# Kernel tuning notes

Measured on AMD Instinct MI355X. Metric: run time of the kernel, lower is better.

## Reference

```python
import jax, jax.numpy as jnp
import numpy as np

NEG_SLOPE = 0.2
EPS = 1e-16

N_NODES = 32768
N_EDGES = 160000
DIM = 768
HEADS1 = 4
OUT1 = DIM // HEADS1  # 192 per head, concat -> 768
HEADS2 = 1
OUT2 = DIM
N_REL = 3


def setup_inputs() -> dict:
    key = jax.random.key(0)
    ks = jax.random.split(key, 12)
    s = 0.02
    return {
        "x": jax.random.normal(ks[0], (N_NODES, DIM), dtype=jnp.float32),
        "edge_index": jax.random.randint(ks[1], (2, N_EDGES), 0, N_NODES, dtype=jnp.int64),
        "edge_type": jax.random.randint(ks[2], (N_EDGES,), 0, N_REL, dtype=jnp.int64),
        "W1": jax.random.normal(ks[3], (N_REL, DIM, HEADS1 * OUT1), dtype=jnp.float32) * s,
        "q1": jax.random.normal(ks[4], (HEADS1 * OUT1, HEADS1), dtype=jnp.float32) * s,
        "k1": jax.random.normal(ks[5], (HEADS1 * OUT1, HEADS1), dtype=jnp.float32) * s,
        "b1": jnp.zeros((HEADS1 * OUT1,), dtype=jnp.float32),
        "W2": jax.random.normal(ks[6], (N_REL, DIM, HEADS2 * OUT2), dtype=jnp.float32) * s,
        "q2": jax.random.normal(ks[7], (HEADS2 * OUT2, HEADS2), dtype=jnp.float32) * s,
        "k2": jax.random.normal(ks[8], (HEADS2 * OUT2, HEADS2), dtype=jnp.float32) * s,
        "b2": jnp.zeros((HEADS2 * OUT2,), dtype=jnp.float32),
    }


def rgat_conv(x, W, q, k, b, src, dst, etype, heads, out_ch, n_nodes):
    """PyG RGATConv, additive-self-attention, across-relation, concat=True, eval mode."""
    # per-relation transform of all nodes: [R, N, H*O] (avoids [E, in, H*O] weight gather)
    xr = jnp.einsum('nd,rdf->rnf', x, W)
    oi = xr[etype, dst]                      # [E, H*O] transformed target feats
    oj = xr[etype, src]                      # [E, H*O] transformed source feats
    qi = oi @ q                              # [E, H]
    kj = oj @ k                              # [E, H]
    alpha = jax.nn.leaky_relu(qi + kj, NEG_SLOPE)
    # segment softmax over edges sharing the same target node
    m = jax.ops.segment_max(alpha, dst, num_segments=n_nodes)     # [N, H]
    e = jnp.exp(alpha - m[dst])
    z = jax.ops.segment_sum(e, dst, num_segments=n_nodes)         # [N, H]
    a = e / (z[dst] + EPS)                                        # [E, H]
    msg = (a[:, :, None] * oj.reshape(-1, heads, out_ch)).reshape(-1, heads * out_ch)
    out = jax.ops.segment_sum(msg, dst, num_segments=n_nodes)     # [N, H*O]
    return out + b


def reference(x, edge_index, edge_type, W1, q1, k1, b1, W2, q2, k2, b2):
    src, dst = edge_index[0], edge_index[1]
    n = x.shape[0]
    h = rgat_conv(x, W1, q1, k1, b1, src, dst, edge_type, HEADS1, OUT1, n)
    h = jax.nn.elu(h)
    # dropout is identity in eval mode
    out = rgat_conv(h, W2, q2, k2, b2, src, dst, edge_type, HEADS2, OUT2, n)
    return out
```

## Files before the change

### kernel.cpp

```cpp
#include <hip/hip_runtime.h>


#define DIM   768
#define NREL  3

typedef __bf16 bf16x8 __attribute__((ext_vector_type(8)));
typedef float  f32x4  __attribute__((ext_vector_type(4)));
typedef unsigned short us4 __attribute__((ext_vector_type(4)));
typedef unsigned short us8 __attribute__((ext_vector_type(8)));

__device__ __forceinline__ float bfs(unsigned short u){
  union { unsigned u; float f; } v; v.u = ((unsigned)u) << 16; return v.f;
}
__device__ __forceinline__ float bfl(unsigned x){
  union { unsigned u; float f; } v; v.u = x << 16; return v.f;
}
__device__ __forceinline__ float bfh(unsigned x){
  union { unsigned u; float f; } v; v.u = x & 0xffff0000u; return v.f;
}
__device__ __forceinline__ unsigned short f2bf(float f){
  union { float f; unsigned u; } v; v.f = f;
  unsigned r = v.u + 0x7fffu + ((v.u >> 16) & 1u);
  return (unsigned short)(r >> 16);
}
__device__ __forceinline__ unsigned pck(float a, float b){
  return (unsigned)f2bf(a) | ((unsigned)f2bf(b) << 16);
}
__device__ __forceinline__ float ldf(const void* p, size_t i, int is32){
  return is32 ? ((const float*)p)[i] : bfs(((const unsigned short*)p)[i]);
}
__device__ __forceinline__ int ldi(const void* p, size_t i, int is64){
  return is64 ? ((const int*)p)[2 * i] : ((const int*)p)[i];
}

typedef __attribute__((address_space(1))) void gvoid_t;
typedef __attribute__((address_space(3))) void lvoid_t;
__device__ __forceinline__ void gload16(const void* g, void* l){
  __builtin_amdgcn_global_load_lds((gvoid_t*)g, (lvoid_t*)l, 16, 0, 0);
}

template<int H>
__device__ __forceinline__ float sel(const float (&a)[H], int h){
  float v = a[0];
#pragma unroll
  for (int i = 1; i < H; ++i) v = (h == i) ? a[i] : v;
  return v;
}

__global__ void detect_kernel(const unsigned short* __restrict__ xu,
                              const unsigned* __restrict__ eiu,
                              const unsigned* __restrict__ etyu,
                              int* __restrict__ flags){
  __shared__ int s_weird, s_ei, s_ety;
  int t = threadIdx.x;
  if (t == 0){ s_weird = 0; s_ei = 0; s_ety = 0; }
  __syncthreads();
  unsigned short u = xu[2 * t];
  int ex = (u >> 7) & 0xff;
  if (ex >= 0xF0 || ex <= 0x40) atomicAdd(&s_weird, 1);
  if (t < 128){
    if (eiu[2 * t + 1]  != 0) atomicAdd(&s_ei, 1);
    if (etyu[2 * t + 1] != 0) atomicAdd(&s_ety, 1);
  }
  __syncthreads();
  if (t == 0){
    flags[0] = (s_weird > 16) ? 1 : 0;
    flags[1] = (s_ei  == 0) ? 1 : 0;
    flags[2] = (s_ety == 0) ? 1 : 0;
  }
}

__global__ void convert_x(const void* __restrict__ xin, unsigned short* __restrict__ xb,
                          const int* __restrict__ flags, int n4){
  int i = blockIdx.x * blockDim.x + threadIdx.x;
  if (i >= n4) return;
  if (flags[0]){
    float4 v = ((const float4*)xin)[i];
    us4 o; o.x = f2bf(v.x); o.y = f2bf(v.y); o.z = f2bf(v.z); o.w = f2bf(v.w);
    ((us4*)xb)[i] = o;
  } else {
    ((us4*)xb)[i] = ((const us4*)xin)[i];
  }
}

__global__ void hist_kernel(const void* __restrict__ ei, int* __restrict__ counts,
                            const int* __restrict__ flags, int E){
  int e = blockIdx.x * blockDim.x + threadIdx.x;
  if (e < E) atomicAdd(&counts[ldi(ei, (size_t)E + e, flags[1])], 1);
}

__global__ void scan_kernel(const int* __restrict__ counts, int* __restrict__ offs,
                            int* __restrict__ cursor, int n){
  __shared__ int s[1024];
  int tid = threadIdx.x;
  int base = tid * 32;
  int loc[32];
  int run = 0;
#pragma unroll
  for (int i = 0; i < 32; ++i){ loc[i] = run; run += counts[base + i]; }
  s[tid] = run;
  __syncthreads();
  for (int off = 1; off < 1024; off <<= 1){
    int add = (tid >= off) ? s[tid - off] : 0;
    __syncthreads();
    s[tid] += add;
    __syncthreads();
  }
  int ex = (tid == 0) ? 0 : s[tid - 1];
#pragma unroll
  for (int i = 0; i < 32; ++i){
    int o = ex + loc[i];
    offs[base + i]   = o;
    cursor[base + i] = o;
  }
  if (tid == 1023) offs[n] = s[1023];
}

__global__ void scatter_kernel(const void* __restrict__ ei, const void* __restrict__ ety,
                               int* __restrict__ cursor, int* __restrict__ payload,
                               const int* __restrict__ flags, int E){
  int e = blockIdx.x * blockDim.x + threadIdx.x;
  if (e < E){
    int dst = ldi(ei, (size_t)E + e, flags[1]);
    int src = ldi(ei, (size_t)e,     flags[1]);
    int et  = ldi(ety, (size_t)e,    flags[2]);
    int pos = atomicAdd(&cursor[dst], 1);
    payload[pos] = (et << 16) | src;
  }
}

__global__ void transpose_w(const void* __restrict__ W, unsigned short* __restrict__ Wt,
                            const int* __restrict__ flags){
  __shared__ unsigned short t[32][33];
  int is32 = flags[0];
  int r = blockIdx.z;
  size_t Wb = (size_t)r * DIM * DIM;
  unsigned short* Wd = Wt + (size_t)r * DIM * DIM;
  int tx = threadIdx.x, ty = threadIdx.y;
  int x  = blockIdx.x * 32 + tx;
  int y0 = blockIdx.y * 32;
#pragma unroll
  for (int i = 0; i < 32; i += 8)
    t[ty + i][tx] = f2bf(ldf(W, Wb + (size_t)(y0 + ty + i) * DIM + x, is32));
  __syncthreads();
  int x2 = blockIdx.y * 32 + tx;
  int y2 = blockIdx.x * 32;
#pragma unroll
  for (int i = 0; i < 32; i += 8) Wd[(size_t)(y2 + ty + i) * DIM + x2] = t[tx][ty + i];
}

template<int H>
__global__ void wqk_kernel(const void* __restrict__ W,
                           const void* __restrict__ q, const void* __restrict__ k,
                           unsigned short* __restrict__ Wqkb,
                           const int* __restrict__ flags){
  int is32 = flags[0];
  int wid  = (blockIdx.x * blockDim.x + threadIdx.x) >> 6;
  int lane = threadIdx.x & 63;
  int r = wid / DIM, d = wid % DIM;
  size_t Wrow = ((size_t)r * DIM + d) * DIM;
  float aq[H], ak[H];
#pragma unroll
  for (int h = 0; h < H; ++h){ aq[h] = 0.f; ak[h] = 0.f; }
#pragma unroll
  for (int j = 0; j < 12; ++j){
    int f = j * 64 + lane;
    float wv = ldf(W, Wrow + f, is32);
#pragma unroll
    for (int h = 0; h < H; ++h){
      aq[h] += wv * ldf(q, (size_t)f * H + h, is32);
      ak[h] += wv * ldf(k, (size_t)f * H + h, is32);
    }
  }
#pragma unroll
  for (int h = 0; h < H; ++h){
    for (int off = 32; off; off >>= 1){
      aq[h] += __shfl_xor(aq[h], off);
      ak[h] += __shfl_xor(ak[h], off);
    }
  }
  if (lane == 0){
#pragma unroll
    for (int h = 0; h < H; ++h){
      Wqkb[(size_t)d * 32 + r * 8 + h]     = f2bf(aq[h]);
      Wqkb[(size_t)d * 32 + r * 8 + 4 + h] = f2bf(ak[h]);
    }
  }
}

__global__ void pack_b(const unsigned short* __restrict__ Wqkb, unsigned short* __restrict__ Bpk){
  int i = blockIdx.x * 256 + threadIdx.x;
  if (i >= 3072) return;
  int lane = i & 63, nt = (i >> 6) & 1, t = i >> 7;
  int kb = t * 32 + (lane >> 4) * 8;
  int col = nt * 16 + (lane & 15);
  us8 v;
#pragma unroll
  for (int j = 0; j < 8; ++j) v[j] = Wqkb[(size_t)(kb + j) * 32 + col];
  ((us8*)Bpk)[i] = v;
}

__global__ void __launch_bounds__(256)
qnkn_mfma(const unsigned short* __restrict__ X, const unsigned short* __restrict__ Bpk,
          float* __restrict__ qn, float* __restrict__ kn, int nN){
  int wv = threadIdx.x >> 6, lane = threadIdx.x & 63;
  int row0 = (blockIdx.x * 4 + wv) * 16;
  int ar = lane & 15, quad = lane >> 4;
  const unsigned short* Arow = X + (size_t)(row0 + ar) * DIM + quad * 8;
  const bf16x8* Bp = (const bf16x8*)Bpk;
  f32x4 acc0 = {0.f,0.f,0.f,0.f}, acc1 = {0.f,0.f,0.f,0.f};
#pragma unroll
  for (int t = 0; t < 24; ++t){
    bf16x8 a  = *(const bf16x8*)(Arow + t * 32);
    bf16x8 b0 = Bp[(t * 2 + 0) * 64 + lane];
    bf16x8 b1 = Bp[(t * 2 + 1) * 64 + lane];
    acc0 = __builtin_amdgcn_mfma_f32_16x16x32_bf16(a, b0, acc0, 0, 0, 0);
    acc1 = __builtin_amdgcn_mfma_f32_16x16x32_bf16(a, b1, acc1, 0, 0, 0);
  }
#pragma unroll
  for (int nt = 0; nt < 2; ++nt){
    int col = nt * 16 + (lane & 15);
    if (col < 24){
      int r = col >> 3, isK = (col >> 2) & 1, h = col & 3;
      float* bp = isK ? kn : qn;
      f32x4 a = nt ? acc1 : acc0;
#pragma unroll
      for (int j = 0; j < 4; ++j){
        int row = row0 + quad * 4 + j;
        bp[((size_t)r * nN + row) * 4 + h] = a[j];
      }
    }
  }
}

#define MM4(mi, av) \
    acc[mi][0] = __builtin_amdgcn_mfma_f32_16x16x32_bf16(av, b0, acc[mi][0], 0, 0, 0); \
    acc[mi][1] = __builtin_amdgcn_mfma_f32_16x16x32_bf16(av, b1, acc[mi][1], 0, 0, 0); \
    acc[mi][2] = __builtin_amdgcn_mfma_f32_16x16x32_bf16(av, b2, acc[mi][2], 0, 0, 0); \
    acc[mi][3] = __builtin_amdgcn_mfma_f32_16x16x32_bf16(av, b3, acc[mi][3], 0, 0, 0);

__global__ void __launch_bounds__(512, 4)
gemm_bf16(const unsigned short* __restrict__ A,
          const unsigned short* __restrict__ Bt,
          unsigned short* __restrict__ C, int M){
  __shared__ __align__(16) unsigned char lds[73728];
  const int K = DIM;
  int i = blockIdx.x;
  int xcd = i & 7, s = i >> 3;
  int bm  = xcd * 32 + s / 9;
  int bnr = s % 9;
  int rrel = bnr / 3, bn = bnr % 3;
  int tid = threadIdx.x;
  int w = tid >> 6, lane = tid & 63;
  int wr = w >> 2, wc = w & 3;
  int m16 = lane & 15, quad = lane >> 4;

  int jlow = m16 >> 1;
  int p    = (((m16 & 1) << 2) | quad) ^ jlow;
  int aoff = (wr * 32 + jlow) * 128 + p * 16;
  int boff = (wc * 32 + jlow) * 128 + p * 16;

  int sq  = (tid & 7) ^ ((tid >> 3) & 7);
  int rb  = 2 * (tid >> 3) + (sq >> 2);
  const unsigned short* gA  = A  + (size_t)(bm * 128 + rb) * K + (sq & 3) * 8;
  const unsigned short* gB0 = Bt + ((size_t)(rrel * DIM + bn * 256 + rb)) * K + (sq & 3) * 8;
  const unsigned short* gB1 = gB0 + (size_t)128 * K;
  unsigned char* dst = &lds[w * 1024];

  f32x4 acc[4][4];
#pragma unroll
  for (int a = 0; a < 4; ++a)
#pragma unroll
    for (int b = 0; b < 4; ++b) acc[a][b] = (f32x4){0.f, 0.f, 0.f, 0.f};

  auto STAGE = [&](int slot, int k0){
    unsigned char* base = dst + slot * 24576;
    gload16(gA  + k0, base);
    gload16(gB0 + k0, base + 8192);
    gload16(gB1 + k0, base + 16384);
  };
  auto LDA = [&](int slot, int mi) -> bf16x8 {
    return *(const bf16x8*)&lds[slot * 24576 + aoff + mi * 1024];
  };
  auto LDB = [&](int slot, int ni) -> bf16x8 {
    return *(const bf16x8*)&lds[slot * 24576 + 8192 + boff + ni * 1024];
  };
  auto PHASE = [&](int slotR, int k0, int slotW, int kW, bool doStage){
    bf16x8 b0 = LDB(slotR, 0), b1 = LDB(slotR, 1), b2 = LDB(slotR, 2), b3 = LDB(slotR, 3);
    bf16x8 a0 = LDA(slotR, 0), a1 = LDA(slotR, 1), a2 = LDA(slotR, 2), a3 = LDA(slotR, 3);
    if (doStage) STAGE(slotW, kW);
    __builtin_amdgcn_s_setprio(1);
    MM4(0, a0) MM4(1, a1) MM4(2, a2) MM4(3, a3)
    __builtin_amdgcn_s_setprio(0);
  };

  STAGE(0, 0); STAGE(1, 32);
  asm volatile("s_waitcnt vmcnt(3)");
  __builtin_amdgcn_s_barrier();

#pragma unroll 1
  for (int t = 0; t < 21; t += 3){
    int k0 = t * 32;
    PHASE(0, k0,       2, k0 + 64, true);
    asm volatile("s_waitcnt vmcnt(3)");
    __builtin_amdgcn_s_barrier();
    PHASE(1, k0 + 32,  0, k0 + 96, true);
    asm volatile("s_waitcnt vmcnt(3)");
    __builtin_amdgcn_s_barrier();
    PHASE(2, k0 + 64,  1, k0 + 128, true);
    asm volatile("s_waitcnt vmcnt(3)");
    __builtin_amdgcn_s_barrier();
  }
  PHASE(0, 672, 2, 736, true);
  asm volatile("s_waitcnt vmcnt(3)");
  __builtin_amdgcn_s_barrier();
  PHASE(1, 704, 0, 0, false);
  asm volatile("s_waitcnt vmcnt(0)");
  __builtin_amdgcn_s_barrier();
  PHASE(2, 736, 0, 0, false);

  unsigned short* Cg = C + ((size_t)rrel * M + (size_t)bm * 128) * DIM + bn * 256;
#pragma unroll
  for (int mi = 0; mi < 4; ++mi)
#pragma unroll
    for (int ni = 0; ni < 4; ++ni){
#pragma unroll
      for (int j = 0; j < 4; ++j){
        int row = wr * 64 + mi * 16 + quad * 4 + j;
        int col = wc * 64 + ni * 16 + m16;
        Cg[(size_t)row * DIM + col] = f2bf(acc[mi][ni][j]);
      }
    }
}

template<int H, bool ELU, bool OUT32>
__global__ void __launch_bounds__(256)
agg_kernel(const unsigned short* __restrict__ xr,
           const float* __restrict__ qn, const float* __restrict__ kn,
           const int* __restrict__ offs, const int* __restrict__ payload,
           const void* __restrict__ bias,
           void* __restrict__ outp,
           const int* __restrict__ flags, int nN, int E){
  const int WH = (H == 4) ? 4 : 1;
  __shared__ int   pay_s[4][64];
  __shared__ float w_s[4][64 * WH];
  int is32 = flags[0];
  int wv   = threadIdx.x >> 6;
  int lane = threadIdx.x & 63;
  int n = blockIdx.x * 4 + wv;
  int rs = offs[n], re = offs[n + 1];
  rs = max(rs, 0); re = min(re, E);
  int hq[3];
#pragma unroll
  for (int q = 0; q < 3; ++q) hq[q] = (H == 1) ? 0 : ((q * 64 + lane) / 48);

  float m_run[H], z_run[H], acc[12];
#pragma unroll
  for (int h = 0; h < H; ++h){ m_run[h] = -__builtin_inff(); z_run[h] = 0.f; }
#pragma unroll
  for (int i = 0; i < 12; ++i) acc[i] = 0.f;

  for (int base = rs; base < re; base += 64){
    int dc = min(64, re - base);
    int pay = 0;
    float al[H];
#pragma unroll
    for (int h = 0; h < H; ++h) al[h] = -__builtin_inff();
    if (lane < dc){
      pay = payload[base + lane];
      int et = pay >> 16, src = pay & 0xffff;
      if (H == 4){
        f32x4 qv = *(const f32x4*)(qn + ((size_t)et * nN + n)   * 4);
        f32x4 kv = *(const f32x4*)(kn + ((size_t)et * nN + src) * 4);
#pragma unroll
        for (int h = 0; h < H; ++h){
          float a = qv[h & 3] + kv[h & 3];
          al[h] = (a > 0.f) ? a : 0.2f * a;
        }
      } else {
        float a = qn[((size_t)et * nN + n) * 4] + kn[((size_t)et * nN + src) * 4];
        al[0] = (a > 0.f) ? a : 0.2f * a;
      }
    }
    float scs[H], wgt[H];
#pragma unroll
    for (int h = 0; h < H; ++h){
      float v = al[h];
      for (int off = 32; off; off >>= 1) v = fmaxf(v, __shfl_xor(v, off));
      float nm = fmaxf(m_run[h], v);
      scs[h] = (m_run[h] == -__builtin_inff()) ? 0.f : expf(m_run[h] - nm);
      m_run[h] = nm;
      wgt[h] = (lane < dc) ? expf(al[h] - nm) : 0.f;
      float s = wgt[h];
      for (int off = 32; off; off >>= 1) s += __shfl_xor(s, off);
      z_run[h] = z_run[h] * scs[h] + s;
    }
#pragma unroll
    for (int q = 0; q < 3; ++q){
      float msc = sel<H>(scs, hq[q]);
#pragma unroll
      for (int j = 0; j < 4; ++j) acc[q * 4 + j] *= msc;
    }

    if (lane < dc){
      pay_s[wv][lane] = pay;
#pragma unroll
      for (int h = 0; h < WH; ++h) w_s[wv][lane * WH + h] = wgt[h];
    }

    for (int j0 = 0; j0 < dc; j0 += 4){
      uint2 c[4][3];
      float w43[4][3];
#pragma unroll
      for (int u = 0; u < 4; ++u){
        int jc = j0 + u;
        int ok = jc < dc;
        int jl = ok ? jc : j0;
        int pj = pay_s[wv][jl];
#pragma unroll
        for (int q = 0; q < 3; ++q){
          float ww = w_s[wv][jl * WH + ((H == 1) ? 0 : hq[q])];
          w43[u][q] = ok ? ww : 0.f;
        }
        int et = pj >> 16, src = pj & 0xffff;
        const uint2* rp = (const uint2*)(xr + ((size_t)et * nN + src) * DIM) + lane;
        c[u][0] = rp[0]; c[u][1] = rp[64]; c[u][2] = rp[128];
      }
#pragma unroll
      for (int u = 0; u < 4; ++u){
#pragma unroll
        for (int q = 0; q < 3; ++q){
          float wj = w43[u][q];
          acc[q * 4 + 0] += wj * bfl(c[u][q].x);
          acc[q * 4 + 1] += wj * bfh(c[u][q].x);
          acc[q * 4 + 2] += wj * bfl(c[u][q].y);
          acc[q * 4 + 3] += wj * bfh(c[u][q].y);
        }
      }
    }
  }

  float o[12];
#pragma unroll
  for (int q = 0; q < 3; ++q){
    float inv = 1.0f / (sel<H>(z_run, hq[q]) + 1e-16f);
#pragma unroll
    for (int j = 0; j < 4; ++j){
      float v = acc[q * 4 + j] * inv + ldf(bias, (size_t)(q * 256 + lane * 4 + j), is32);
      if (ELU) v = (v > 0.f) ? v : (expf(v) - 1.f);
      o[q * 4 + j] = v;
    }
  }
  if (OUT32 && is32){
    float* op = (float*)outp + (size_t)n * DIM + lane * 4;
    ((float4*)(op      ))[0] = (float4){o[0], o[1], o[2],  o[3]};
    ((float4*)(op + 256))[0] = (float4){o[4], o[5], o[6],  o[7]};
    ((float4*)(op + 512))[0] = (float4){o[8], o[9], o[10], o[11]};
  } else {
    unsigned short* ob = (unsigned short*)outp + (size_t)n * DIM + lane * 4;
    uint2 s0, s1, s2;
    s0.x = pck(o[0], o[1]);  s0.y = pck(o[2],  o[3]);
    s1.x = pck(o[4], o[5]);  s1.y = pck(o[6],  o[7]);
    s2.x = pck(o[8], o[9]);  s2.y = pck(o[10], o[11]);
    *(uint2*)(ob      ) = s0;
    *(uint2*)(ob + 256) = s1;
    *(uint2*)(ob + 512) = s2;
  }
}

extern "C" void kernel_launch(void* const* d_in, const int* in_sizes, int n_in,
                              void* d_out, int out_size, void* d_ws, size_t ws_size,
                              hipStream_t stream){
  const void* x   = d_in[0];
  const void* ei  = d_in[1];
  const void* ety = d_in[2];
  const void* W1  = d_in[3];
  const void* q1  = d_in[4];
  const void* k1  = d_in[5];
  const void* b1  = d_in[6];
  const void* W2  = d_in[7];
  const void* q2  = d_in[8];
  const void* k2  = d_in[9];
  const void* b2  = d_in[10];

  int nN = in_sizes[0] / DIM;
  int E  = in_sizes[2];

  char* ws = (char*)d_ws;
  size_t off = 0;
  auto alloc = [&](size_t bytes) -> void* {
    void* p = ws + off;
    off += (bytes + 255) & ~(size_t)255;
    return p;
  };
  unsigned short* xr   = (unsigned short*)alloc((size_t)NREL * nN * DIM * 2);
  unsigned short* xb   = (unsigned short*)alloc((size_t)nN * DIM * 2);
  unsigned short* h    = (unsigned short*)alloc((size_t)nN * DIM * 2);
  unsigned short* Wt   = (unsigned short*)alloc((size_t)NREL * DIM * DIM * 2);
  unsigned short* Wqkb = (unsigned short*)alloc((size_t)DIM * 32 * 2);
  unsigned short* Bpk  = (unsigned short*)alloc((size_t)3072 * 16);
  float* qn  = (float*)alloc((size_t)NREL * nN * 4 * 4);
  float* kn  = (float*)alloc((size_t)NREL * nN * 4 * 4);
  int* offs    = (int*)alloc((size_t)(nN + 1) * 4);
  int* cursor  = (int*)alloc((size_t)nN * 4);
  int* counts  = (int*)alloc((size_t)nN * 4);
  int* payload = (int*)alloc((size_t)E * 4);
  int* flags   = (int*)alloc(16);

  detect_kernel<<<1, 256, 0, stream>>>((const unsigned short*)x, (const unsigned*)ei,
                                       (const unsigned*)ety, flags);
  convert_x<<<(nN * DIM / 4 + 255) / 256, 256, 0, stream>>>(x, xb, flags, nN * DIM / 4);

  hipMemsetAsync(counts, 0, (size_t)nN * 4, stream);
  hist_kernel<<<(E + 255) / 256, 256, 0, stream>>>(ei, counts, flags, E);
  scan_kernel<<<1, 1024, 0, stream>>>(counts, offs, cursor, nN);
  scatter_kernel<<<(E + 255) / 256, 256, 0, stream>>>(ei, ety, cursor, payload, flags, E);

  dim3 tg(DIM / 32, DIM / 32, NREL), tb(32, 8);
  int gemm_blocks = 8 * (32 * 9);

  transpose_w<<<tg, tb, 0, stream>>>(W1, Wt, flags);
  hipMemsetAsync(Wqkb, 0, (size_t)DIM * 32 * 2, stream);
  wqk_kernel<4><<<(NREL * DIM) / 4, 256, 0, stream>>>(W1, q1, k1, Wqkb, flags);
  pack_b<<<12, 256, 0, stream>>>(Wqkb, Bpk);
  qnkn_mfma<<<nN / 64, 256, 0, stream>>>(xb, Bpk, qn, kn, nN);
  gemm_bf16<<<gemm_blocks, 512, 0, stream>>>(xb, Wt, xr, nN);
  agg_kernel<4, true, false><<<nN / 4, 256, 0, stream>>>(xr, qn, kn, offs, payload, b1, h,
                                                         flags, nN, E);

  transpose_w<<<tg, tb, 0, stream>>>(W2, Wt, flags);
  hipMemsetAsync(Wqkb, 0, (size_t)DIM * 32 * 2, stream);
  wqk_kernel<1><<<(NREL * DIM) / 4, 256, 0, stream>>>(W2, q2, k2, Wqkb, flags);
  pack_b<<<12, 256, 0, stream>>>(Wqkb, Bpk);
  qnkn_mfma<<<nN / 64, 256, 0, stream>>>(h, Bpk, qn, kn, nN);
  gemm_bf16<<<gemm_blocks, 512, 0, stream>>>(h, Wt, xr, nN);
  agg_kernel<1, false, true><<<nN / 4, 256, 0, stream>>>(xr, qn, kn, offs, payload, b2,
                                                         d_out, flags, nN, E);
}
```

Baseline: 658.2 us.

## Fuse attention q/k projection MFMA into the relation GEMM to reuse A tiles

```diff
diff --git a/kernel.cpp b/kernel.cpp
--- a/kernel.cpp
+++ b/kernel.cpp
@@ -200,49 +200,44 @@
   ((us8*)Bpk)[i] = v;
 }
 
-__global__ void __launch_bounds__(256)
-qnkn_mfma(const unsigned short* __restrict__ X, const unsigned short* __restrict__ Bpk,
-          float* __restrict__ qn, float* __restrict__ kn, int nN){
-  int wv = threadIdx.x >> 6, lane = threadIdx.x & 63;
-  int row0 = (blockIdx.x * 4 + wv) * 16;
-  int ar = lane & 15, quad = lane >> 4;
-  const unsigned short* Arow = X + (size_t)(row0 + ar) * DIM + quad * 8;
-  const bf16x8* Bp = (const bf16x8*)Bpk;
-  f32x4 acc0 = {0.f,0.f,0.f,0.f}, acc1 = {0.f,0.f,0.f,0.f};
-#pragma unroll
-  for (int t = 0; t < 24; ++t){
-    bf16x8 a  = *(const bf16x8*)(Arow + t * 32);
-    bf16x8 b0 = Bp[(t * 2 + 0) * 64 + lane];
-    bf16x8 b1 = Bp[(t * 2 + 1) * 64 + lane];
-    acc0 = __builtin_amdgcn_mfma_f32_16x16x32_bf16(a, b0, acc0, 0, 0, 0);
-    acc1 = __builtin_amdgcn_mfma_f32_16x16x32_bf16(a, b1, acc1, 0, 0, 0);
-  }
-#pragma unroll
-  for (int nt = 0; nt < 2; ++nt){
-    int col = nt * 16 + (lane & 15);
-    if (col < 24){
-      int r = col >> 3, isK = (col >> 2) & 1, h = col & 3;
-      float* bp = isK ? kn : qn;
-      f32x4 a = nt ? acc1 : acc0;
-#pragma unroll
-      for (int j = 0; j < 4; ++j){
-        int row = row0 + quad * 4 + j;
-        bp[((size_t)r * nN + row) * 4 + h] = a[j];
-      }
-    }
-  }
-}
-
 #define MM4(mi, av) \
     acc[mi][0] = __builtin_amdgcn_mfma_f32_16x16x32_bf16(av, b0, acc[mi][0], 0, 0, 0); \
     acc[mi][1] = __builtin_amdgcn_mfma_f32_16x16x32_bf16(av, b1, acc[mi][1], 0, 0, 0); \
     acc[mi][2] = __builtin_amdgcn_mfma_f32_16x16x32_bf16(av, b2, acc[mi][2], 0, 0, 0); \
     acc[mi][3] = __builtin_amdgcn_mfma_f32_16x16x32_bf16(av, b3, acc[mi][3], 0, 0, 0);
 
+#define MFQ(A_, B_, C_) __builtin_amdgcn_mfma_f32_16x16x32_bf16(A_, B_, C_, 0, 0, 0)
+
+#define STEPQ(SL, PAR, NPAR, T, DOST, DOLBQ) {                                \
+  if ((DOLBQ) && qkOn){                                                       \
+    bqs##NPAR##x[0] = Bpv[((T) + 1) * 128 + lane];                            \
+    bqs##NPAR##x[1] = Bpv[((T) + 1) * 128 + 64 + lane];                       \
+  }                                                                           \
+  if (DOST) STAGE((SL + 2) % 3, ((T) + 2) * 32);                              \
+  bf16x8 b0 = LDB(SL, 0), b1 = LDB(SL, 1), b2 = LDB(SL, 2), b3 = LDB(SL, 3);  \
+  bf16x8 a0 = LDA(SL, 0), a1 = LDA(SL, 1), a2 = LDA(SL, 2), a3 = LDA(SL, 3);  \
+  __builtin_amdgcn_s_setprio(1);                                              \
+  MM4(0, a0) MM4(1, a1) MM4(2, a2) MM4(3, a3)                                 \
+  if (qkOn){                                                                  \
+    aqk[0][0] = MFQ(a0, bqs##PAR##x[0], aqk[0][0]);                           \
+    aqk[0][1] = MFQ(a0, bqs##PAR##x[1], aqk[0][1]);                           \
+    aqk[1][0] = MFQ(a1, bqs##PAR##x[0], aqk[1][0]);                           \
+    aqk[1][1] = MFQ(a1, bqs##PAR##x[1], aqk[1][1]);                           \
+    aqk[2][0] = MFQ(a2, bqs##PAR##x[0], aqk[2][0]);                           \
+    aqk[2][1] = MFQ(a2, bqs##PAR##x[1], aqk[2][1]);                           \
+    aqk[3][0] = MFQ(a3, bqs##PAR##x[0], aqk[3][0]);                           \
+    aqk[3][1] = MFQ(a3, bqs##PAR##x[1], aqk[3][1]);                           \
+  }                                                                           \
+  __builtin_amdgcn_s_setprio(0);                                              \
+}
+#define W3 { asm volatile("s_waitcnt vmcnt(3)"); __builtin_amdgcn_s_barrier(); }
+
 __global__ void __launch_bounds__(512, 4)
 gemm_bf16(const unsigned short* __restrict__ A,
           const unsigned short* __restrict__ Bt,
-          unsigned short* __restrict__ C, int M){
+          unsigned short* __restrict__ C,
+          const unsigned short* __restrict__ Bpk,
+          float* __restrict__ qn, float* __restrict__ kn, int M){
   __shared__ __align__(16) unsigned char lds[73728];
   const int K = DIM;
   int i = blockIdx.x;
@@ -254,6 +249,7 @@
   int w = tid >> 6, lane = tid & 63;
   int wr = w >> 2, wc = w & 3;
   int m16 = lane & 15, quad = lane >> 4;
+  int qkOn = (bnr == 0) && (wc == 0);
 
   int jlow = m16 >> 1;
   int p    = (((m16 & 1) << 2) | quad) ^ jlow;
@@ -266,12 +262,17 @@
   const unsigned short* gB0 = Bt + ((size_t)(rrel * DIM + bn * 256 + rb)) * K + (sq & 3) * 8;
   const unsigned short* gB1 = gB0 + (size_t)128 * K;
   unsigned char* dst = &lds[w * 1024];
+  const bf16x8* Bpv = (const bf16x8*)Bpk;
 
   f32x4 acc[4][4];
 #pragma unroll
   for (int a = 0; a < 4; ++a)
 #pragma unroll
     for (int b = 0; b < 4; ++b) acc[a][b] = (f32x4){0.f, 0.f, 0.f, 0.f};
+  f32x4 aqk[4][2];
+#pragma unroll
+  for (int a = 0; a < 4; ++a){ aqk[a][0] = (f32x4){0.f,0.f,0.f,0.f}; aqk[a][1] = (f32x4){0.f,0.f,0.f,0.f}; }
+  bf16x8 bqs0x[2], bqs1x[2];
 
   auto STAGE = [&](int slot, int k0){
     unsigned char* base = dst + slot * 24576;
@@ -285,39 +286,28 @@
   auto LDB = [&](int slot, int ni) -> bf16x8 {
     return *(const bf16x8*)&lds[slot * 24576 + 8192 + boff + ni * 1024];
   };
-  auto PHASE = [&](int slotR, int k0, int slotW, int kW, bool doStage){
-    bf16x8 b0 = LDB(slotR, 0), b1 = LDB(slotR, 1), b2 = LDB(slotR, 2), b3 = LDB(slotR, 3);
-    bf16x8 a0 = LDA(slotR, 0), a1 = LDA(slotR, 1), a2 = LDA(slotR, 2), a3 = LDA(slotR, 3);
-    if (doStage) STAGE(slotW, kW);
-    __builtin_amdgcn_s_setprio(1);
-    MM4(0, a0) MM4(1, a1) MM4(2, a2) MM4(3, a3)
-    __builtin_amdgcn_s_setprio(0);
-  };
-
+
+  if (qkOn){ bqs0x[0] = Bpv[lane]; bqs0x[1] = Bpv[64 + lane]; }
   STAGE(0, 0); STAGE(1, 32);
-  asm volatile("s_waitcnt vmcnt(3)");
-  __builtin_amdgcn_s_barrier();
+  W3;
 
 #pragma unroll 1
-  for (int t = 0; t < 21; t += 3){
-    int k0 = t * 32;
-    PHASE(0, k0,       2, k0 + 64, true);
-    asm volatile("s_waitcnt vmcnt(3)");
-    __builtin_amdgcn_s_barrier();
-    PHASE(1, k0 + 32,  0, k0 + 96, true);
-    asm volatile("s_waitcnt vmcnt(3)");
-    __builtin_amdgcn_s_barrier();
-    PHASE(2, k0 + 64,  1, k0 + 128, true);
-    asm volatile("s_waitcnt vmcnt(3)");
-    __builtin_amdgcn_s_barrier();
-  }
-  PHASE(0, 672, 2, 736, true);
-  asm volatile("s_waitcnt vmcnt(3)");
-  __builtin_amdgcn_s_barrier();
-  PHASE(1, 704, 0, 0, false);
+  for (int t6 = 0; t6 < 18; t6 += 6){
+    STEPQ(0, 0, 1, t6 + 0, 1, 1) W3;
+    STEPQ(1, 1, 0, t6 + 1, 1, 1) W3;
+    STEPQ(2, 0, 1, t6 + 2, 1, 1) W3;
+    STEPQ(0, 1, 0, t6 + 3, 1, 1) W3;
+    STEPQ(1, 0, 1, t6 + 4, 1, 1) W3;
+    STEPQ(2, 1, 0, t6 + 5, 1, 1) W3;
+  }
+  STEPQ(0, 0, 1, 18, 1, 1) W3;
+  STEPQ(1, 1, 0, 19, 1, 1) W3;
+  STEPQ(2, 0, 1, 20, 1, 1) W3;
+  STEPQ(0, 1, 0, 21, 1, 1) W3;
+  STEPQ(1, 0, 1, 22, 0, 1)
   asm volatile("s_waitcnt vmcnt(0)");
   __builtin_amdgcn_s_barrier();
-  PHASE(2, 736, 0, 0, false);
+  STEPQ(2, 1, 0, 23, 0, 0)
 
   unsigned short* Cg = C + ((size_t)rrel * M + (size_t)bm * 128) * DIM + bn * 256;
 #pragma unroll
@@ -331,6 +321,24 @@
         Cg[(size_t)row * DIM + col] = f2bf(acc[mi][ni][j]);
       }
     }
+
+  if (qkOn){
+#pragma unroll
+    for (int mi = 0; mi < 4; ++mi)
+#pragma unroll
+      for (int nt = 0; nt < 2; ++nt){
+        int col = nt * 16 + m16;
+        if (col < 24){
+          int r = col >> 3, isK = (col >> 2) & 1, h = col & 3;
+          float* bp = isK ? kn : qn;
+#pragma unroll
+          for (int j = 0; j < 4; ++j){
+            int row = bm * 128 + wr * 64 + mi * 16 + quad * 4 + j;
+            bp[((size_t)r * M + row) * 4 + h] = aqk[mi][nt][j];
+          }
+        }
+      }
+  }
 }
 
 template<int H, bool ELU, bool OUT32>
@@ -498,7 +506,7 @@
   unsigned short* h    = (unsigned short*)alloc((size_t)nN * DIM * 2);
   unsigned short* Wt   = (unsigned short*)alloc((size_t)NREL * DIM * DIM * 2);
   unsigned short* Wqkb = (unsigned short*)alloc((size_t)DIM * 32 * 2);
-  unsigned short* Bpk  = (unsigned short*)alloc((size_t)3072 * 16);
+  unsigned short* Bpk  = (unsigned short*)alloc((size_t)3200 * 16);
   float* qn  = (float*)alloc((size_t)NREL * nN * 4 * 4);
   float* kn  = (float*)alloc((size_t)NREL * nN * 4 * 4);
   int* offs    = (int*)alloc((size_t)(nN + 1) * 4);
@@ -523,8 +531,7 @@
   hipMemsetAsync(Wqkb, 0, (size_t)DIM * 32 * 2, stream);
   wqk_kernel<4><<<(NREL * DIM) / 4, 256, 0, stream>>>(W1, q1, k1, Wqkb, flags);
   pack_b<<<12, 256, 0, stream>>>(Wqkb, Bpk);
-  qnkn_mfma<<<nN / 64, 256, 0, stream>>>(xb, Bpk, qn, kn, nN);
-  gemm_bf16<<<gemm_blocks, 512, 0, stream>>>(xb, Wt, xr, nN);
+  gemm_bf16<<<gemm_blocks, 512, 0, stream>>>(xb, Wt, xr, Bpk, qn, kn, nN);
   agg_kernel<4, true, false><<<nN / 4, 256, 0, stream>>>(xr, qn, kn, offs, payload, b1, h,
                                                          flags, nN, E);
 
@@ -532,8 +539,7 @@
   hipMemsetAsync(Wqkb, 0, (size_t)DIM * 32 * 2, stream);
   wqk_kernel<1><<<(NREL * DIM) / 4, 256, 0, stream>>>(W2, q2, k2, Wqkb, flags);
   pack_b<<<12, 256, 0, stream>>>(Wqkb, Bpk);
-  qnkn_mfma<<<nN / 64, 256, 0, stream>>>(h, Bpk, qn, kn, nN);
-  gemm_bf16<<<gemm_blocks, 512, 0, stream>>>(h, Wt, xr, nN);
+  gemm_bf16<<<gemm_blocks, 512, 0, stream>>>(h, Wt, xr, Bpk, qn, kn, nN);
   agg_kernel<1, false, true><<<nN / 4, 256, 0, stream>>>(xr, qn, kn, offs, payload, b2,
                                                          d_out, flags, nN, E);
 }
```

Measured after the change: 1.172 ms. 1.78x slower.
